# Kernel optimization log

Measured on AMD Instinct MI355X. Metric: run time of the kernel, lower is better.

## Reference

```python
import jax, jax.numpy as jnp
import numpy as np

B, J, O = 32, 20, 20
D, H, F, L = 256, 8, 1024, 6
S = J * O
DH = D // H
NL = L + 1  # 6 encoder blocks + final block stacked together


def setup_inputs() -> dict:
    ks = jax.random.split(jax.random.key(0), 16)
    s = 0.02
    am = jax.random.randint(ks[4], (B, J), 0, 2) == 1
    am = am.at[:, 0].set(False)  # at least one unmasked job per row (avoid all -inf softmax)
    return {
        "operations": jax.random.normal(ks[0], (B, J, O, 2), jnp.float32),
        "job_ops_mask": jax.random.normal(ks[1], (B, J, O, O), jnp.float32),
        "ops_machines_mask": jax.random.normal(ks[2], (B, S, S), jnp.float32),
        "jobs_next_op_idx": jax.random.randint(ks[3], (B, J, 1), 0, O),
        "action_mask": am,
        "qkv_w": jax.random.normal(ks[5], (NL, 3 * D, D), jnp.float32) * s,
        "qkv_b": jnp.zeros((NL, 3 * D), jnp.float32),
        "out_w": jax.random.normal(ks[6], (NL, D, D), jnp.float32) * s,
        "out_b": jnp.zeros((NL, D), jnp.float32),
        "ln1_g": jnp.ones((NL, D), jnp.float32),
        "ln1_b": jnp.zeros((NL, D), jnp.float32),
        "ln2_g": jnp.ones((NL, D), jnp.float32),
        "ln2_b": jnp.zeros((NL, D), jnp.float32),
        "ff1_w": jax.random.normal(ks[7], (NL, F, D), jnp.float32) * s,
        "ff1_b": jnp.zeros((NL, F), jnp.float32),
        "ff2_w": jax.random.normal(ks[8], (NL, D, F), jnp.float32) * s,
        "ff2_b": jnp.zeros((NL, D), jnp.float32),
        "op_emb_w": jax.random.normal(ks[9], (D, 2), jnp.float32) * s,
        "op_emb_b": jnp.zeros((D,), jnp.float32),
        "pol_w": jax.random.normal(ks[10], (1, D), jnp.float32) * s,
        "pol_b": jnp.zeros((1,), jnp.float32),
    }


def _ln(x, g, b):
    m = x.mean(-1, keepdims=True)
    v = ((x - m) ** 2).mean(-1, keepdims=True)
    return (x - m) * jax.lax.rsqrt(v + 1e-5) * g + b


def _mha(x, mask, qw, qb, ow, ob):
    N, Sq, _ = x.shape
    qkv = x @ qw.T + qb
    q, k, v = jnp.split(qkv, 3, axis=-1)
    q = q.reshape(N, Sq, H, DH).transpose(0, 2, 1, 3)
    k = k.reshape(N, Sq, H, DH).transpose(0, 2, 1, 3)
    v = v.reshape(N, Sq, H, DH).transpose(0, 2, 1, 3)
    sc = jnp.einsum("nhqd,nhkd->nhqk", q, k) / jnp.sqrt(jnp.float32(DH))
    sc = sc + mask  # additive float attn mask, broadcast over heads where needed
    a = jax.nn.softmax(sc, axis=-1)
    o = jnp.einsum("nhqk,nhkd->nhqd", a, v).transpose(0, 2, 1, 3).reshape(N, Sq, D)
    return o @ ow.T + ob


def _forward(operations, job_ops_mask, ops_machines_mask, jobs_next_op_idx, action_mask,
             qkv_w, qkv_b, out_w, out_b, ln1_g, ln1_b, ln2_g, ln2_b,
             ff1_w, ff1_b, ff2_w, ff2_b, op_emb_w, op_emb_b, pol_w, pol_b):
    def block(x, mask, i):  # pre-norm TransformerEncoderLayer, gelu, dropout=0
        h = _ln(x, ln1_g[i], ln1_b[i])
        x = x + _mha(h, mask, qkv_w[i], qkv_b[i], out_w[i], out_b[i])
        h = _ln(x, ln2_g[i], ln2_b[i])
        ff = jax.nn.gelu(h @ ff1_w[i].T + ff1_b[i], approximate=False) @ ff2_w[i].T + ff2_b[i]
        return x + ff

    # sinusoidal positional encoding over the operation index
    pos = jnp.arange(O, dtype=jnp.float32)[:, None]
    div = jnp.exp(jnp.arange(0, D, 2, dtype=jnp.float32) * (-np.log(10000.0) / D))
    pe = jnp.stack([jnp.sin(pos * div), jnp.cos(pos * div)], axis=-1).reshape(O, D)
    x = operations @ op_emb_w.T + op_emb_b + pe[None, None]  # (B,J,O,D)

    # ALiBi slopes: 1/x^(i+1), x = 256^(1/H)
    base = (2.0 ** 8) ** (1.0 / H)
    slope = (1.0 / base ** jnp.arange(1, H + 1, dtype=jnp.float32))[None, :, None, None]
    job_mask = job_ops_mask.reshape(B * J, 1, O, O) * slope  # (B*J, H, O, O)
    mach_mask = ops_machines_mask[:, None, :, :]  # (B, 1, S, S), identical across heads

    for i in range(L):
        if i % 2 == 0:  # per-job attention over operations
            x = block(x.reshape(B * J, O, D), job_mask, i).reshape(B, J, O, D)
        else:  # per-machine attention over all operations
            x = block(x.reshape(B, S, D), mach_mask, i).reshape(B, J, O, D)

    idx = jnp.broadcast_to(jobs_next_op_idx[:, :, :, None], (B, J, 1, D))
    nxt = jnp.take_along_axis(x, idx, axis=2)[:, :, 0, :]  # (B, J, D)
    kp = jnp.where(action_mask, -jnp.inf, 0.0)[:, None, None, :]  # key padding mask
    nxt = block(nxt, kp, L)
    logits = (nxt @ pol_w.T + pol_b)[:, :, 0]
    return jnp.where(action_mask, -jnp.inf, logits)


def reference(operations, job_ops_mask, ops_machines_mask, jobs_next_op_idx, action_mask,
              qkv_w, qkv_b, out_w, out_b, ln1_g, ln1_b, ln2_g, ln2_b,
              ff1_w, ff1_b, ff2_w, ff2_b, op_emb_w, op_emb_b, pol_w, pol_b):
    return _forward(operations, job_ops_mask, ops_machines_mask, jobs_next_op_idx, action_mask,
                    qkv_w, qkv_b, out_w, out_b, ln1_g, ln1_b, ln2_g, ln2_b,
                    ff1_w, ff1_b, ff2_w, ff2_b, op_emb_w, op_emb_b, pol_w, pol_b)
```

## Files before the change

### kernel.cpp

```cpp
#include <hip/hip_runtime.h>
#include <math.h>

#define B_  32
#define J_  20
#define O_  20
#define S_  400
#define D_  256
#define H_  8
#define F_  1024
#define L_  6
#define T_  12800
#define T2_ 640

#define NEG_BIG (-1e30f)

typedef __attribute__((ext_vector_type(8))) short short8;
typedef __attribute__((ext_vector_type(4))) float f32x4;

__device__ __forceinline__ short f2b(float f) {
  union { float f; unsigned u; } c; c.f = f;
  unsigned r = (c.u + 0x7FFFu + ((c.u >> 16) & 1u)) >> 16;
  return (short)r;
}
__device__ __forceinline__ float b2f(short s) {
  union { unsigned u; float f; } c;
  c.u = ((unsigned)(unsigned short)s) << 16;
  return c.f;
}
__device__ __forceinline__ unsigned addpk(unsigned a, unsigned b) {
  union { unsigned u; float f; } x, y;
  x.u = a << 16;        y.u = b << 16;        float lo = x.f + y.f;
  x.u = a & 0xffff0000u; y.u = b & 0xffff0000u; float hi = x.f + y.f;
  return (unsigned)(unsigned short)f2b(lo) | ((unsigned)(unsigned short)f2b(hi) << 16);
}
__device__ __forceinline__ void async_copy16(const short* g, short* l) {
  __builtin_amdgcn_global_load_lds(
      (const __attribute__((address_space(1))) void*)g,
      (__attribute__((address_space(3))) void*)l, 16, 0, 0);
}

__global__ __launch_bounds__(256) void k_f2b4(
    const float* __restrict__ s0, short* __restrict__ d0,
    const float* __restrict__ s1, short* __restrict__ d1,
    const float* __restrict__ s2, short* __restrict__ d2,
    const float* __restrict__ s3, short* __restrict__ d3)
{
  int bid = blockIdx.x;
  const float* src; short* dst; int base;
  if (bid < 672)        { src = s0; dst = d0; base = bid; }
  else if (bid < 896)   { src = s1; dst = d1; base = bid - 672; }
  else if (bid < 1792)  { src = s2; dst = d2; base = bid - 896; }
  else                  { src = s3; dst = d3; base = bid - 1792; }
  int i = (base * 256 + threadIdx.x) * 8;
  float4 a = *(const float4*)(src + i);
  float4 b = *(const float4*)(src + i + 4);
  short8 o;
  o[0] = f2b(a.x); o[1] = f2b(a.y); o[2] = f2b(a.z); o[3] = f2b(a.w);
  o[4] = f2b(b.x); o[5] = f2b(b.y); o[6] = f2b(b.z); o[7] = f2b(b.w);
  *(short8*)(dst + i) = o;
}

__global__ __launch_bounds__(640) void k_maskconv(
    const void* __restrict__ am_raw, int* __restrict__ am_out)
{
  __shared__ int isInt32;
  const int tid = threadIdx.x;
  if (tid == 0) isInt32 = 1;
  __syncthreads();
  if (tid < 160) {
    int v = ((const int*)am_raw)[tid];
    if (v != 0 && v != 1) atomicAnd(&isInt32, 0);
  }
  __syncthreads();
  if (tid < 640) {
    int v;
    if (isInt32) v = ((const int*)am_raw)[tid] != 0;
    else         v = ((const unsigned char*)am_raw)[tid] != 0;
    am_out[tid] = v;
  }
}

__global__ __launch_bounds__(256) void k_embed(
    const float* __restrict__ ops, const float* __restrict__ ew,
    const float* __restrict__ eb, short* __restrict__ x)
{
  int idx = blockIdx.x * 256 + threadIdx.x;
  int d = idx & 255;
  int t = idx >> 8;
  int o = t % O_;
  float a0 = ops[(size_t)t * 2 + 0], a1 = ops[(size_t)t * 2 + 1];
  int k = d >> 1;
  float div = expf((float)(2 * k) * -0.03597789207803197f);
  float ang = (float)o * div;
  float pe = (d & 1) ? cosf(ang) : sinf(ang);
  x[idx] = f2b(a0 * ew[d * 2 + 0] + a1 * ew[d * 2 + 1] + eb[d] + pe);
}

__global__ __launch_bounds__(256) void k_ln(
    const short* __restrict__ x, const float* __restrict__ g, const float* __restrict__ b,
    short* __restrict__ out, int nTok)
{
  int gid = blockIdx.x * 256 + threadIdx.x;
  int tok = gid >> 6, lane = threadIdx.x & 63;
  if (tok >= nTok) return;
  int2 pk = ((const int2*)(x + (size_t)tok * 256))[lane];
  union { unsigned u; float f; } c;
  float vx, vy, vz, vw;
  c.u = (unsigned)pk.x << 16;        vx = c.f;
  c.u = (unsigned)pk.x & 0xffff0000u; vy = c.f;
  c.u = (unsigned)pk.y << 16;        vz = c.f;
  c.u = (unsigned)pk.y & 0xffff0000u; vw = c.f;
  float s = vx + vy + vz + vw;
  #pragma unroll
  for (int off = 32; off > 0; off >>= 1) s += __shfl_down(s, off);
  float mean = __shfl(s, 0) * (1.f / 256.f);
  float dx = vx - mean, dy = vy - mean, dz = vz - mean, dw = vw - mean;
  float q = dx * dx + dy * dy + dz * dz + dw * dw;
  #pragma unroll
  for (int off = 32; off > 0; off >>= 1) q += __shfl_down(q, off);
  float var = __shfl(q, 0) * (1.f / 256.f);
  float inv = 1.f / sqrtf(var + 1e-5f);
  float4 gv = ((const float4*)g)[lane];
  float4 bv = ((const float4*)b)[lane];
  float ox = dx * inv * gv.x + bv.x;
  float oy = dy * inv * gv.y + bv.y;
  float oz = dz * inv * gv.z + bv.z;
  float ow = dw * inv * gv.w + bv.w;
  int2 po;
  po.x = (int)(unsigned short)f2b(ox) | ((int)(unsigned short)f2b(oy) << 16);
  po.y = (int)(unsigned short)f2b(oz) | ((int)(unsigned short)f2b(ow) << 16);
  ((int2*)(out + (size_t)tok * 256))[lane] = po;
}

__global__ __launch_bounds__(256) void k_gemm_bf16(
    const short* __restrict__ A, const short* __restrict__ W,
    const float* __restrict__ bias, const short* __restrict__ R,
    short* __restrict__ C, int M, int N, int K, int act)
{
  __shared__ short LDS_[17408];
  short* Asf = LDS_;
  short* Bsf = LDS_ + 8192;
  short* Csf = LDS_;
  const int tid  = threadIdx.x;
  const int lane = tid & 63;
  const int wv   = tid >> 6;
  const int lm   = lane & 15;
  const int quad = lane >> 4;
  const int wm   = (wv >> 1) * 64;
  const int wn   = (wv & 1) * 64;
  const int n0 = blockIdx.x * 128;
  const int m0 = blockIdx.y * 128;

  f32x4 acc[4][4] = {};

  for (int k0 = 0; k0 < K; k0 += 64) {
    __syncthreads();
    #pragma unroll
    for (int i = 0; i < 4; ++i) {
      const int c    = tid + 256 * i;
      const int row  = c >> 3;
      const int kc8  = ((c & 7) ^ (row & 7)) * 8;
      async_copy16(A + (size_t)(m0 + row) * K + k0 + kc8, &Asf[c * 8]);
      async_copy16(W + (size_t)(n0 + row) * K + k0 + kc8, &Bsf[c * 8]);
    }
    __syncthreads();
    #pragma unroll
    for (int kh = 0; kh < 2; ++kh) {
      short8 af[4], bf[4];
      #pragma unroll
      for (int i = 0; i < 4; ++i) {
        const int row  = wm + i * 16 + lm;
        const int slot = (kh * 4 + quad) ^ (lm & 7);
        af[i] = *(short8*)&Asf[(row * 8 + slot) * 8];
      }
      #pragma unroll
      for (int j = 0; j < 4; ++j) {
        const int row  = wn + j * 16 + lm;
        const int slot = (kh * 4 + quad) ^ (lm & 7);
        bf[j] = *(short8*)&Bsf[(row * 8 + slot) * 8];
      }
      #pragma unroll
      for (int i = 0; i < 4; ++i)
        #pragma unroll
        for (int j = 0; j < 4; ++j)
          acc[i][j] = __builtin_amdgcn_mfma_f32_16x16x32_bf16(af[i], bf[j], acc[i][j], 0, 0, 0);
    }
  }

  __syncthreads();
  #pragma unroll
  for (int j = 0; j < 4; ++j) {
    const int ccol = wn + j * 16 + lm;
    const float bv = bias[n0 + ccol];
    #pragma unroll
    for (int i = 0; i < 4; ++i) {
      #pragma unroll
      for (int r = 0; r < 4; ++r) {
        const int row = wm + i * 16 + quad * 4 + r;
        float vvv = acc[i][j][r] + bv;
        if (act) vvv = vvv / (1.f + __expf(-1.702f * vvv));
        Csf[row * 136 + ccol] = f2b(vvv);
      }
    }
  }
  __syncthreads();
  {
    const int srow = tid >> 1, sh = (tid & 1) * 64;
    const size_t gbase = (size_t)(m0 + srow) * N + n0 + sh;
    const short* ls = &Csf[srow * 136 + sh];
    #pragma unroll
    for (int u = 0; u < 8; ++u) {
      uint4 v = *(const uint4*)(ls + u * 8);
      if (R) {
        uint4 rv = *(const uint4*)(R + gbase + u * 8);
        v.x = addpk(v.x, rv.x); v.y = addpk(v.y, rv.y);
        v.z = addpk(v.z, rv.z); v.w = addpk(v.w, rv.w);
      }
      *(uint4*)(C + gbase + u * 8) = v;
    }
  }
}

__global__ __launch_bounds__(256) void k_gemm_ln(
    const short* __restrict__ A, const short* __restrict__ W,
    const float* __restrict__ bias, const short* __restrict__ R,
    short* __restrict__ X, short* __restrict__ Hout,
    const float* __restrict__ g, const float* __restrict__ bb_,
    int M, int K)
{
  __shared__ short LDS_[4096 + 16896];
  short* Asf = LDS_;
  short* Bsf = LDS_ + 4096;
  short* Csf = LDS_ + 4096;
  const int tid  = threadIdx.x;
  const int lane = tid & 63;
  const int wv   = tid >> 6;
  const int lm   = lane & 15;
  const int quad = lane >> 4;
  const int wn   = wv * 64;
  const int m0   = blockIdx.x * 64;

  f32x4 acc[4][4] = {};

  for (int k0 = 0; k0 < K; k0 += 64) {
    __syncthreads();
    #pragma unroll
    for (int i = 0; i < 2; ++i) {
      const int c   = tid + 256 * i;
      const int row = c >> 3;
      const int kc8 = ((c & 7) ^ (row & 7)) * 8;
      async_copy16(A + (size_t)(m0 + row) * K + k0 + kc8, &Asf[c * 8]);
    }
    #pragma unroll
    for (int i = 0; i < 8; ++i) {
      const int c   = tid + 256 * i;
      const int row = c >> 3;
      const int kc8 = ((c & 7) ^ (row & 7)) * 8;
      async_copy16(W + (size_t)row * K + k0 + kc8, &Bsf[c * 8]);
    }
    __syncthreads();
    #pragma unroll
    for (int kh = 0; kh < 2; ++kh) {
      short8 af[4], bf[4];
      #pragma unroll
      for (int i = 0; i < 4; ++i) {
        const int row  = i * 16 + lm;
        const int slot = (kh * 4 + quad) ^ (lm & 7);
        af[i] = *(short8*)&Asf[(row * 8 + slot) * 8];
      }
      #pragma unroll
      for (int j = 0; j < 4; ++j) {
        const int row  = wn + j * 16 + lm;
        const int slot = (kh * 4 + quad) ^ (lm & 7);
        bf[j] = *(short8*)&Bsf[(row * 8 + slot) * 8];
      }
      #pragma unroll
      for (int i = 0; i < 4; ++i)
        #pragma unroll
        for (int j = 0; j < 4; ++j)
          acc[i][j] = __builtin_amdgcn_mfma_f32_16x16x32_bf16(af[i], bf[j], acc[i][j], 0, 0, 0);
    }
  }

  __syncthreads();
  #pragma unroll
  for (int j = 0; j < 4; ++j) {
    const int ccol = wn + j * 16 + lm;
    const float bv = bias[ccol];
    #pragma unroll
    for (int i = 0; i < 4; ++i) {
      #pragma unroll
      for (int r = 0; r < 4; ++r) {
        const int row = i * 16 + quad * 4 + r;
        Csf[row * 264 + ccol] = f2b(acc[i][j][r] + bv);
      }
    }
  }
  __syncthreads();

  {
    const int row = tid >> 2, cb = (tid & 3) * 64;
    const size_t gbase = (size_t)(m0 + row) * 256 + cb;
    const short* ls = &Csf[row * 264 + cb];
    uint4 xv[8];
    float s1 = 0.f, s2 = 0.f;
    #pragma unroll
    for (int u = 0; u < 8; ++u) {
      uint4 v = *(const uint4*)(ls + u * 8);
      uint4 rv = *(const uint4*)(R + gbase + u * 8);
      v.x = addpk(v.x, rv.x); v.y = addpk(v.y, rv.y);
      v.z = addpk(v.z, rv.z); v.w = addpk(v.w, rv.w);
      xv[u] = v;
      *(uint4*)(X + gbase + u * 8) = v;
      #pragma unroll
      for (int w2 = 0; w2 < 4; ++w2) {
        unsigned pv = (&v.x)[w2];
        union { unsigned u; float f; } c1, c2;
        c1.u = pv << 16; c2.u = pv & 0xffff0000u;
        s1 += c1.f + c2.f;
        s2 += c1.f * c1.f + c2.f * c2.f;
      }
    }
    s1 += __shfl_xor(s1, 1); s2 += __shfl_xor(s2, 1);
    s1 += __shfl_xor(s1, 2); s2 += __shfl_xor(s2, 2);
    const float mean = s1 * (1.f / 256.f);
    const float var  = s2 * (1.f / 256.f) - mean * mean;
    const float inv  = 1.f / sqrtf(var + 1e-5f);
    #pragma unroll
    for (int u = 0; u < 8; ++u) {
      float4 g0 = *(const float4*)(g + cb + u * 8);
      float4 g1 = *(const float4*)(g + cb + u * 8 + 4);
      float4 b0 = *(const float4*)(bb_ + cb + u * 8);
      float4 b1 = *(const float4*)(bb_ + cb + u * 8 + 4);
      auto lnpk = [&](unsigned pv, float ga, float gb2, float ba, float bb2) -> unsigned {
        union { unsigned u; float f; } c1, c2;
        c1.u = pv << 16; c2.u = pv & 0xffff0000u;
        float lo = (c1.f - mean) * inv * ga + ba;
        float hi = (c2.f - mean) * inv * gb2 + bb2;
        return (unsigned)(unsigned short)f2b(lo) | ((unsigned)(unsigned short)f2b(hi) << 16);
      };
      uint4 hv;
      hv.x = lnpk(xv[u].x, g0.x, g0.y, b0.x, b0.y);
      hv.y = lnpk(xv[u].y, g0.z, g0.w, b0.z, b0.w);
      hv.z = lnpk(xv[u].z, g1.x, g1.y, b1.x, b1.y);
      hv.w = lnpk(xv[u].w, g1.z, g1.w, b1.z, b1.w);
      *(uint4*)(Hout + gbase + u * 8) = hv;
    }
  }
}

#define QSTR 776
#define PSTR20 40
__global__ __launch_bounds__(512) void k_attn20_mfma(
    const short* __restrict__ qkv, short* __restrict__ att,
    const float* __restrict__ jmask, const int* __restrict__ amask, int mode)
{
  __shared__ short QK[32 * QSTR];
  __shared__ short Ps[8][32 * PSTR20];
  const int seq  = blockIdx.x;
  const int tid  = threadIdx.x;
  const int wv   = tid >> 6;
  const int lane = tid & 63;
  const int l15  = lane & 15;
  const int quad = lane >> 4;
  const float scale = 0.1767766952966369f;

  for (int e = tid; e < 3072; e += 512) {
    int row = e / 96, c8 = (e % 96) * 8;
    uint4 v = {0u, 0u, 0u, 0u};
    if (row < 20) v = *(const uint4*)(qkv + ((size_t)seq * 20 + row) * 768 + c8);
    *(uint4*)&QK[row * QSTR + c8] = v;
  }
  __syncthreads();

  const short8 aq0 = *(short8*)&QK[(0  + l15) * QSTR + wv * 32 + quad * 8];
  const short8 aq1 = *(short8*)&QK[(16 + l15) * QSTR + wv * 32 + quad * 8];
  const short8 bk0 = *(short8*)&QK[(0  + l15) * QSTR + 256 + wv * 32 + quad * 8];
  const short8 bk1 = *(short8*)&QK[(16 + l15) * QSTR + 256 + wv * 32 + quad * 8];
  f32x4 z4 = {0.f, 0.f, 0.f, 0.f};
  f32x4 s00 = __builtin_amdgcn_mfma_f32_16x16x32_bf16(aq0, bk0, z4, 0, 0, 0);
  f32x4 s01 = __builtin_amdgcn_mfma_f32_16x16x32_bf16(aq0, bk1, z4, 0, 0, 0);
  f32x4 s10 = __builtin_amdgcn_mfma_f32_16x16x32_bf16(aq1, bk0, z4, 0, 0, 0);
  f32x4 s11 = __builtin_amdgcn_mfma_f32_16x16x32_bf16(aq1, bk1, z4, 0, 0, 0);

  const float slope = exp2f(-(float)(wv + 1));
  short* psw = &Ps[wv][0];
  float l0[4] = {0.f, 0.f, 0.f, 0.f};
  float l1[4] = {0.f, 0.f, 0.f, 0.f};

  #pragma unroll
  for (int kt = 0; kt < 2; ++kt) {
    const int k  = kt * 16 + l15;
    const int kc = (k < 20) ? k : 19;
    float madd1 = 0.f;
    if (mode == 1) madd1 = amask[seq * 20 + kc] ? NEG_BIG : 0.f;
    #pragma unroll
    for (int qt = 0; qt < 2; ++qt) {
      f32x4 s = (kt == 0) ? (qt == 0 ? s00 : s10) : (qt == 0 ? s01 : s11);
      #pragma unroll
      for (int r = 0; r < 4; ++r) {
        const int q  = qt * 16 + quad * 4 + r;
        const int qc = (q < 20) ? q : 19;
        float sv = s[r] * scale;
        if (mode == 0) sv += jmask[(size_t)seq * 400 + qc * 20 + kc] * slope;
        else           sv += madd1;
        float p = (k < 20) ? __expf(fminf(sv, 40.f)) : 0.f;
        if (qt == 0) l0[r] += p; else l1[r] += p;
        psw[q * PSTR20 + k] = f2b(p);
      }
    }
  }
  #pragma unroll
  for (int r = 0; r < 4; ++r) {
    float t0 = l0[r];
    t0 += __shfl_xor(t0, 1); t0 += __shfl_xor(t0, 2);
    t0 += __shfl_xor(t0, 4); t0 += __shfl_xor(t0, 8);
    l0[r] = 1.f / t0;
    float t1 = l1[r];
    t1 += __shfl_xor(t1, 1); t1 += __shfl_xor(t1, 2);
    t1 += __shfl_xor(t1, 4); t1 += __shfl_xor(t1, 8);
    l1[r] = 1.f / t1;
  }

  const short8 pf0 = *(short8*)&psw[(0  + l15) * PSTR20 + quad * 8];
  const short8 pf1 = *(short8*)&psw[(16 + l15) * PSTR20 + quad * 8];
  #pragma unroll
  for (int dt = 0; dt < 2; ++dt) {
    const int d = wv * 32 + dt * 16 + l15;
    short8 vf;
    #pragma unroll
    for (int j = 0; j < 8; ++j)
      vf[j] = QK[(quad * 8 + j) * QSTR + 512 + d];
    f32x4 o0 = __builtin_amdgcn_mfma_f32_16x16x32_bf16(pf0, vf, z4, 0, 0, 0);
    f32x4 o1 = __builtin_amdgcn_mfma_f32_16x16x32_bf16(pf1, vf, z4, 0, 0, 0);
    #pragma unroll
    for (int r = 0; r < 4; ++r) {
      const int q = quad * 4 + r;
      att[((size_t)seq * 20 + q) * 256 + d] = f2b(o0[r] * l0[r]);
    }
    if (quad == 0) {
      #pragma unroll
      for (int r = 0; r < 4; ++r) {
        const int q = 16 + r;
        att[((size_t)seq * 20 + q) * 256 + d] = f2b(o1[r] * l1[r]);
      }
    }
  }
}

#define VSTR 36
#define PSTRW 40
__global__ __launch_bounds__(512) void k_attn400_mfma(
    const short* __restrict__ qkv, short* __restrict__ att,
    const float* __restrict__ mmask)
{
  __shared__ short Wl[8 * 1792];

  const int id   = blockIdx.x;
  const int b    = (id >> 3) / 25 * 8 + (id & 7);
  const int qt   = (id >> 3) % 25;
  const int tid  = threadIdx.x;
  const int wv   = tid >> 6;
  const int lane = tid & 63;
  const int l15  = lane & 15;
  const int quad = lane >> 4;
  const int q0   = qt * 16;
  const float scale = 0.1767766952966369f;

  short* Vw = &Wl[wv * 1792];
  short* Pw = &Wl[wv * 1792 + 1152];
  const short* qbase = qkv + (size_t)b * 400 * 768;

  const short8 af = *(const short8*)(qbase + (size_t)(q0 + l15) * 768 + wv * 32 + quad * 8);

  f32x4 accO[2] = {};
  float lrun[4] = {0.f, 0.f, 0.f, 0.f};
  const float* mrow_base = mmask + ((size_t)b * 400 + q0) * 400;

  const int vrow = lane >> 1;
  const int vch  = (lane & 1) * 2;
  const int vdst = vrow * VSTR + vch * 8;

  short8 kf0, kf1;
  float mA[4], mB[4];
  auto prefKM = [&](int k0) {
    kf0 = *(const short8*)(qbase + (size_t)(k0 + l15) * 768 + 256 + wv * 32 + quad * 8);
    kf1 = *(const short8*)(qbase + (size_t)(k0 + 16 + l15) * 768 + 256 + wv * 32 + quad * 8);
    const int kA = k0 + l15, kB = k0 + 16 + l15;
    #pragma unroll
    for (int r = 0; r < 4; ++r) {
      const int qrow = quad * 4 + r;
      mA[r] = mrow_base[(size_t)qrow * 400 + kA];
      mB[r] = (kB < 400) ? mrow_base[(size_t)qrow * 400 + kB] : 0.f;
    }
  };
  prefKM(0);

  for (int k0 = 0; k0 < 416; k0 += 32) {
    const short* vp = qbase + (size_t)(k0 + vrow) * 768 + 512 + wv * 32 + vch * 8;
    const uint4 v0 = *(const uint4*)vp;
    const uint4 v1 = *(const uint4*)(vp + 8);

    const short8 ck0 = kf0, ck1 = kf1;
    float cA[4], cB[4];
    #pragma unroll
    for (int r = 0; r < 4; ++r) { cA[r] = mA[r]; cB[r] = mB[r]; }

    f32x4 z4 = {0.f, 0.f, 0.f, 0.f};
    f32x4 s0 = __builtin_amdgcn_mfma_f32_16x16x32_bf16(af, ck0, z4, 0, 0, 0);
    f32x4 s1 = __builtin_amdgcn_mfma_f32_16x16x32_bf16(af, ck1, z4, 0, 0, 0);

    if (k0 + 32 < 416) prefKM(k0 + 32);

    const int kB = k0 + 16 + l15;
    float p0[4], p1[4];
    #pragma unroll
    for (int r = 0; r < 4; ++r) {
      float svA = s0[r] * scale + cA[r];
      float svB = (kB < 400) ? (s1[r] * scale + cB[r]) : NEG_BIG;
      p0[r] = __expf(fminf(svA, 40.f));
      p1[r] = __expf(fminf(svB, 40.f));
      lrun[r] += p0[r] + p1[r];
    }

    #pragma unroll
    for (int r = 0; r < 4; ++r) {
      const int qrow = quad * 4 + r;
      Pw[qrow * PSTRW + l15]      = f2b(p0[r]);
      Pw[qrow * PSTRW + 16 + l15] = f2b(p1[r]);
    }
    const short8 pf = *(short8*)&Pw[l15 * PSTRW + quad * 8];

    *(uint4*)&Vw[vdst]     = v0;
    *(uint4*)&Vw[vdst + 8] = v1;
    #pragma unroll
    for (int c = 0; c < 2; ++c) {
      short8 vf;
      #pragma unroll
      for (int j = 0; j < 8; ++j)
        vf[j] = Vw[(quad * 8 + j) * VSTR + c * 16 + l15];
      accO[c] = __builtin_amdgcn_mfma_f32_16x16x32_bf16(pf, vf, accO[c], 0, 0, 0);
    }
  }

  #pragma unroll
  for (int r = 0; r < 4; ++r) {
    float t = lrun[r];
    t += __shfl_xor(t, 1);
    t += __shfl_xor(t, 2);
    t += __shfl_xor(t, 4);
    t += __shfl_xor(t, 8);
    lrun[r] = t;
  }

  #pragma unroll
  for (int c = 0; c < 2; ++c) {
    const int dcol = wv * 32 + c * 16 + l15;
    #pragma unroll
    for (int r = 0; r < 4; ++r) {
      float o = accO[c][r] / lrun[r];
      att[((size_t)b * 400 + q0 + quad * 4 + r) * 256 + dcol] = f2b(o);
    }
  }
}

__global__ __launch_bounds__(256) void k_gather2(
    const short* __restrict__ x, const short* __restrict__ h,
    const int* __restrict__ idx, short* __restrict__ x2, short* __restrict__ h2)
{
  int t = blockIdx.x * 256 + threadIdx.x;
  if (t >= 640 * 16) return;
  int bj = t >> 4, c = t & 15;
  int o = idx[bj];
  size_t src = ((size_t)bj * 20 + o) * 256;
  ((uint4*)(x2 + (size_t)bj * 256))[c] = ((const uint4*)(x + src))[c];
  ((uint4*)(h2 + (size_t)bj * 256))[c] = ((const uint4*)(h + src))[c];
}

__global__ __launch_bounds__(256) void k_logits(
    const short* __restrict__ x2, const float* __restrict__ pw, const float* __restrict__ pb,
    const int* __restrict__ am, float* __restrict__ out)
{
  int gid = blockIdx.x * 256 + threadIdx.x;
  int row = gid >> 6, lane = threadIdx.x & 63;
  int2 pk = ((const int2*)(x2 + (size_t)row * 256))[lane];
  union { unsigned u; float f; } c;
  float vx, vy, vz, vw;
  c.u = (unsigned)pk.x << 16;         vx = c.f;
  c.u = (unsigned)pk.x & 0xffff0000u; vy = c.f;
  c.u = (unsigned)pk.y << 16;         vz = c.f;
  c.u = (unsigned)pk.y & 0xffff0000u; vw = c.f;
  float4 w = ((const float4*)pw)[lane];
  float s = vx * w.x + vy * w.y + vz * w.z + vw * w.w;
  #pragma unroll
  for (int off = 32; off > 0; off >>= 1) s += __shfl_down(s, off);
  if (lane == 0) out[row] = am[row] ? NEG_BIG : (s + pb[0]);
}

extern "C" void kernel_launch(void* const* d_in, const int* in_sizes, int n_in,
                              void* d_out, int out_size, void* d_ws, size_t ws_size,
                              hipStream_t stream)
{
  (void)in_sizes; (void)n_in; (void)out_size; (void)ws_size;
  const float* operations        = (const float*)d_in[0];
  const float* job_ops_mask      = (const float*)d_in[1];
  const float* ops_machines_mask = (const float*)d_in[2];
  const int*   jobs_next_op_idx  = (const int*)d_in[3];
  const void*  action_mask_raw   = (const void*)d_in[4];
  const float* qkv_w = (const float*)d_in[5];
  const float* qkv_b = (const float*)d_in[6];
  const float* out_w = (const float*)d_in[7];
  const float* out_b = (const float*)d_in[8];
  const float* ln1_g = (const float*)d_in[9];
  const float* ln1_b = (const float*)d_in[10];
  const float* ln2_g = (const float*)d_in[11];
  const float* ln2_b = (const float*)d_in[12];
  const float* ff1_w = (const float*)d_in[13];
  const float* ff1_b = (const float*)d_in[14];
  const float* ff2_w = (const float*)d_in[15];
  const float* ff2_b = (const float*)d_in[16];
  const float* op_emb_w = (const float*)d_in[17];
  const float* op_emb_b = (const float*)d_in[18];
  const float* pol_w = (const float*)d_in[19];
  const float* pol_b = (const float*)d_in[20];
  float* out = (float*)d_out;

  short* x    = (short*)d_ws;
  short* x2   = x + (size_t)T_ * D_;
  short* h    = x2 + (size_t)T2_ * D_;
  short* big  = h + (size_t)T_ * D_;
  short* h2   = big + (size_t)T_ * F_;
  short* big2 = h2 + (size_t)T2_ * D_;
  int*   amc  = (int*)(big2 + (size_t)T2_ * F_);
  short* bwq  = (short*)(amc + 640);
  short* bwo  = bwq + (size_t)7 * 768 * 256;
  short* bwf1 = bwo + (size_t)7 * 256 * 256;
  short* bwf2 = bwf1 + (size_t)7 * 1024 * 256;

  auto gemm = [&](const short* A, const short* Wb, const float* bias, const short* R,
                  short* C, int M, int N, int K, int act) {
    k_gemm_bf16<<<dim3(N / 128, M / 128), dim3(256), 0, stream>>>(
        A, Wb, bias, R, C, M, N, K, act);
  };
  auto gemm_ln = [&](const short* A, const short* Wb, const float* bias, const short* R,
                     short* X, short* Hout, const float* g, const float* b, int M, int K) {
    k_gemm_ln<<<dim3(M / 64), dim3(256), 0, stream>>>(
        A, Wb, bias, R, X, Hout, g, b, M, K);
  };

  k_f2b4<<<dim3(2688), 256, 0, stream>>>(qkv_w, bwq, out_w, bwo, ff1_w, bwf1, ff2_w, bwf2);
  k_maskconv<<<dim3(1), dim3(640), 0, stream>>>(action_mask_raw, amc);
  k_embed<<<dim3(T_ * D_ / 256), dim3(256), 0, stream>>>(operations, op_emb_w, op_emb_b, x);
  k_ln<<<dim3(T_ / 4), 256, 0, stream>>>(x, ln1_g, ln1_b, h, T_);

  for (int i = 0; i < L_; ++i) {
    const short* qw  = bwq  + (size_t)i * 768 * 256;
    const float* qb  = qkv_b + (size_t)i * 768;
    const short* ow  = bwo  + (size_t)i * 256 * 256;
    const float* ob  = out_b + (size_t)i * 256;
    const short* f1w = bwf1 + (size_t)i * 1024 * 256;
    const float* f1b = ff1_b + (size_t)i * 1024;
    const short* f2w = bwf2 + (size_t)i * 256 * 1024;
    const float* f2b_ = ff2_b + (size_t)i * 256;
    gemm(h, qw, qb, nullptr, big, T_, 768, 256, 0);
    if ((i & 1) == 0)
      k_attn20_mfma<<<dim3(640), 512, 0, stream>>>(big, h, job_ops_mask, nullptr, 0);
    else
      k_attn400_mfma<<<dim3(800), 512, 0, stream>>>(big, h, ops_machines_mask);
    gemm_ln(h, ow, ob, x, x, h, ln2_g + i * D_, ln2_b + i * D_, T_, 256);
    gemm(h, f1w, f1b, nullptr, big, T_, 1024, 256, 1);
    gemm_ln(big, f2w, f2b_, x, x, h, ln1_g + (i + 1) * D_, ln1_b + (i + 1) * D_, T_, 1024);
  }

  k_gather2<<<dim3(40), 256, 0, stream>>>(x, h, jobs_next_op_idx, x2, h2);

  {
    int i = L_;
    const short* qw  = bwq  + (size_t)i * 768 * 256;
    const float* qb  = qkv_b + (size_t)i * 768;
    const short* ow  = bwo  + (size_t)i * 256 * 256;
    const float* ob  = out_b + (size_t)i * 256;
    const short* f1w = bwf1 + (size_t)i * 1024 * 256;
    const float* f1b = ff1_b + (size_t)i * 1024;
    const short* f2w = bwf2 + (size_t)i * 256 * 1024;
    const float* f2b_ = ff2_b + (size_t)i * 256;
    gemm(h2, qw, qb, nullptr, big2, T2_, 768, 256, 0);
    k_attn20_mfma<<<dim3(32), 512, 0, stream>>>(big2, h2, nullptr, amc, 1);
    gemm_ln(h2, ow, ob, x2, x2, h2, ln2_g + i * D_, ln2_b + i * D_, T2_, 256);
    gemm(h2, f1w, f1b, nullptr, big2, T2_, 1024, 256, 1);
    gemm(big2, f2w, f2b_, x2, x2, T2_, 256, 1024, 0);
  }

  k_logits<<<dim3(160), 256, 0, stream>>>(x2, pol_w, pol_b, amc, out);
}
```

Baseline: 984.6 us.

## Load GEMM MFMA fragments directly from global memory, bypassing LDS staging

The bf16 GEMM kernel no longer stages A and W tiles through shared memory with async copies and barriers. Each wave now reads its MFMA operand fragments straight from global memory, stepping 32 along K with a 2x unroll. This removes the per-tile barriers and LDS round trips, but drops the reuse that shared tiles gave between waves, so each operand is fetched once per wave pair and relies on L1/L2 caching. The global loads are 16-byte row-strided accesses, which may coalesce poorly.

```diff
diff --git a/kernel.cpp b/kernel.cpp
--- a/kernel.cpp
+++ b/kernel.cpp
@@ -137,10 +137,7 @@
     const float* __restrict__ bias, const short* __restrict__ R,
     short* __restrict__ C, int M, int N, int K, int act)
 {
-  __shared__ short LDS_[17408];
-  short* Asf = LDS_;
-  short* Bsf = LDS_ + 8192;
-  short* Csf = LDS_;
+  __shared__ short Csf[128 * 136];
   const int tid  = threadIdx.x;
   const int lane = tid & 63;
   const int wv   = tid >> 6;
@@ -151,43 +148,28 @@
   const int n0 = blockIdx.x * 128;
   const int m0 = blockIdx.y * 128;
 
+  const short* Abase = A + (size_t)(m0 + wm + lm) * K + quad * 8;
+  const short* Wbase = W + (size_t)(n0 + wn + lm) * K + quad * 8;
+  const size_t rstep16 = (size_t)16 * K;
+
   f32x4 acc[4][4] = {};
 
-  for (int k0 = 0; k0 < K; k0 += 64) {
-    __syncthreads();
-    #pragma unroll
-    for (int i = 0; i < 4; ++i) {
-      const int c    = tid + 256 * i;
-      const int row  = c >> 3;
-      const int kc8  = ((c & 7) ^ (row & 7)) * 8;
-      async_copy16(A + (size_t)(m0 + row) * K + k0 + kc8, &Asf[c * 8]);
-      async_copy16(W + (size_t)(n0 + row) * K + k0 + kc8, &Bsf[c * 8]);
-    }
-    __syncthreads();
-    #pragma unroll
-    for (int kh = 0; kh < 2; ++kh) {
-      short8 af[4], bf[4];
-      #pragma unroll
-      for (int i = 0; i < 4; ++i) {
-        const int row  = wm + i * 16 + lm;
-        const int slot = (kh * 4 + quad) ^ (lm & 7);
-        af[i] = *(short8*)&Asf[(row * 8 + slot) * 8];
-      }
-      #pragma unroll
-      for (int j = 0; j < 4; ++j) {
-        const int row  = wn + j * 16 + lm;
-        const int slot = (kh * 4 + quad) ^ (lm & 7);
-        bf[j] = *(short8*)&Bsf[(row * 8 + slot) * 8];
-      }
-      #pragma unroll
-      for (int i = 0; i < 4; ++i)
-        #pragma unroll
-        for (int j = 0; j < 4; ++j)
-          acc[i][j] = __builtin_amdgcn_mfma_f32_16x16x32_bf16(af[i], bf[j], acc[i][j], 0, 0, 0);
-    }
-  }
-
-  __syncthreads();
+  #pragma unroll 2
+  for (int k0 = 0; k0 < K; k0 += 32) {
+    short8 af[4], bf[4];
+    #pragma unroll
+    for (int i = 0; i < 4; ++i)
+      af[i] = *(const short8*)(Abase + i * rstep16 + k0);
+    #pragma unroll
+    for (int j = 0; j < 4; ++j)
+      bf[j] = *(const short8*)(Wbase + j * rstep16 + k0);
+    #pragma unroll
+    for (int i = 0; i < 4; ++i)
+      #pragma unroll
+      for (int j = 0; j < 4; ++j)
+        acc[i][j] = __builtin_amdgcn_mfma_f32_16x16x32_bf16(af[i], bf[j], acc[i][j], 0, 0, 0);
+  }
+
   #pragma unroll
   for (int j = 0; j < 4; ++j) {
     const int ccol = wn + j * 16 + lm;
```

After: 1.148 ms. 1.17x slower.
